# Performance work log

Hardware: AMD Instinct MI355X
Metric: run time of the kernel (lower is better)

The kernel has to match this reference:

```python
import jax, jax.numpy as jnp
import numpy as np

NUM_GRAPHS = 512


def _sage_conv(x, src, tgt, num_nodes, w_n, b_n, w_r):
    # PyG SAGEConv with mean aggregation:
    #   out = mean_{j in N(i)} x_j @ w_n + b_n + x_i @ w_r
    msgs = x[src]                                   # [E, d] gather
    agg = jax.ops.segment_sum(msgs, tgt, num_segments=num_nodes)   # [N, d]
    deg = jax.ops.segment_sum(jnp.ones((src.shape[0],), x.dtype), tgt,
                              num_segments=num_nodes)              # [N]
    agg = agg / jnp.maximum(deg, 1.0)[:, None]
    return agg @ w_n + b_n + x @ w_r


def setup_inputs() -> dict:
    key = jax.random.key(0)
    ks = jax.random.split(key, 10)
    N, E, D_IN, D_H, D_OUT = 50000, 800000, 128, 128, 10
    s = 0.05
    x = jax.random.normal(ks[0], (N, D_IN), dtype=jnp.float32)
    edge_index = jax.random.randint(ks[1], (2, E), 0, N, dtype=jnp.int64)
    batch = jnp.sort(jax.random.randint(ks[2], (N,), 0, NUM_GRAPHS, dtype=jnp.int64))
    return {
        "x": x,
        "edge_index": edge_index,
        "batch": batch,
        "w1_n": jax.random.normal(ks[3], (D_IN, D_H), dtype=jnp.float32) * s,
        "b1": jnp.zeros((D_H,), jnp.float32),
        "w1_r": jax.random.normal(ks[4], (D_IN, D_H), dtype=jnp.float32) * s,
        "w2_n": jax.random.normal(ks[5], (D_H, D_H), dtype=jnp.float32) * s,
        "b2": jnp.zeros((D_H,), jnp.float32),
        "w2_r": jax.random.normal(ks[6], (D_H, D_H), dtype=jnp.float32) * s,
        "fc_w": jax.random.normal(ks[7], (D_H, D_OUT), dtype=jnp.float32) * s,
        "fc_b": jnp.zeros((D_OUT,), jnp.float32),
    }


def reference(x, edge_index, batch, w1_n, b1, w1_r, w2_n, b2, w2_r, fc_w, fc_b):
    N = x.shape[0]
    src, tgt = edge_index[0], edge_index[1]
    h = _sage_conv(x, src, tgt, N, w1_n, b1, w1_r)
    h = jax.nn.relu(h)  # dropout is identity in eval mode
    h = _sage_conv(h, src, tgt, N, w2_n, b2, w2_r)
    # global_mean_pool over graph ids
    pooled = jax.ops.segment_sum(h, batch, num_segments=NUM_GRAPHS)
    cnt = jax.ops.segment_sum(jnp.ones((N,), h.dtype), batch, num_segments=NUM_GRAPHS)
    pooled = pooled / jnp.maximum(cnt, 1.0)[:, None]
    return pooled @ fc_w + fc_b
```

## Files before the change

kernel.cpp:

```cpp
#include <hip/hip_runtime.h>

#define D 128
#define G_NUM 512

typedef unsigned short u16;
typedef unsigned int u32;
typedef __attribute__((ext_vector_type(8))) short bf16x8;
typedef __attribute__((ext_vector_type(4))) float f32x4;

__device__ __forceinline__ float bf2f(u16 u) {
    return __uint_as_float(((u32)u) << 16);
}
__device__ __forceinline__ u16 f2bf_rne(float f) {
    u32 u = __float_as_uint(f);
    u32 r = (u + 0x7FFFu + ((u >> 16) & 1u)) >> 16;
    return (u16)r;
}
__device__ __forceinline__ void split_bf16(float v, u16& h, u16& l) {
    h = f2bf_rne(v);
    l = f2bf_rne(v - bf2f(h));
}
__device__ __forceinline__ float pk_hi(u32 u) { return __uint_as_float(u & 0xFFFF0000u); }
__device__ __forceinline__ float pk_lo(u32 u) { return __uint_as_float(u << 16); }
__device__ __forceinline__ bf16x8 mk8(u32 a, u32 b, u32 c, u32 d) {
    union { u32 u[4]; bf16x8 v; } t;
    t.u[0] = a; t.u[1] = b; t.u[2] = c; t.u[3] = d;
    return t.v;
}

__global__ void prep_kernel(const float* __restrict__ x, u16* __restrict__ xh, u16* __restrict__ xl,
                            const float* __restrict__ w0, const float* __restrict__ w1,
                            const float* __restrict__ w2, const float* __restrict__ w3,
                            u16* __restrict__ wp,
                            const int* __restrict__ batch, int* __restrict__ gstart,
                            const int* __restrict__ tgt, int* __restrict__ deg,
                            int n4, int E, int N, int NBX, int NBE) {
    int b = blockIdx.x, t = threadIdx.x;
    if (b < NBX) {
        int i = b * 256 + t;
        if (i >= n4) return;
        float4 v = ((const float4*)x)[i];
        ushort4 h, l;
        split_bf16(v.x, h.x, l.x);
        split_bf16(v.y, h.y, l.y);
        split_bf16(v.z, h.z, l.z);
        split_bf16(v.w, h.w, l.w);
        ((ushort4*)xh)[i] = h;
        ((ushort4*)xl)[i] = l;
    } else if (b < NBX + NBE) {
        int e = (b - NBX) * 256 + t;
        if (e < E) atomicAdd(&deg[tgt[e]], 1);
    } else if (b < NBX + NBE + 32) {
        int id = (b - NBX - NBE) * 256 + t;
        int g = id & 3, c = (id >> 2) & 127, kt = (id >> 9) & 3, mat = id >> 11;
        const float* W = (mat == 0) ? w0 : (mat == 1) ? w1 : (mat == 2) ? w2 : w3;
        u16* dh = wp + mat * 32768 + ((size_t)(kt * 128 + c) * 4 + g) * 8;
        u16* dl = dh + 16384;
#pragma unroll
        for (int j = 0; j < 8; j++) {
            float v = W[(size_t)(kt * 32 + g * 8 + j) * D + c];
            u16 h, l;
            split_bf16(v, h, l);
            dh[j] = h;
            dl[j] = l;
        }
    } else {
        int i = (b - NBX - NBE - 32) * 256 + t;
        if (i >= N) return;
        int bb = batch[i];
        int bp = (i == 0) ? -1 : batch[i - 1];
        for (int g = bp + 1; g <= bb; g++) gstart[g] = i;
        if (i == N - 1)
            for (int g = bb + 1; g <= G_NUM; g++) gstart[g] = N;
    }
}

__global__ void scan1_kernel(const int* __restrict__ deg, int* __restrict__ row_excl,
                             int* __restrict__ partial, int N) {
    __shared__ int s[256];
    int t = threadIdx.x, i = blockIdx.x * 256 + t;
    int v = (i < N) ? deg[i] : 0;
    s[t] = v;
    __syncthreads();
    for (int off = 1; off < 256; off <<= 1) {
        int add = (t >= off) ? s[t - off] : 0;
        __syncthreads();
        s[t] += add;
        __syncthreads();
    }
    if (i < N) row_excl[i] = s[t] - v;
    if (t == 255) partial[blockIdx.x] = s[255];
}

__global__ void scan2_kernel(int* __restrict__ partial, int NB) {
    __shared__ int s[256];
    int t = threadIdx.x;
    int v = (t < NB) ? partial[t] : 0;
    s[t] = v;
    __syncthreads();
    for (int off = 1; off < 256; off <<= 1) {
        int add = (t >= off) ? s[t - off] : 0;
        __syncthreads();
        s[t] += add;
        __syncthreads();
    }
    if (t < NB) partial[t] = s[t] - v;
}

__global__ void scan3_kernel(int* __restrict__ row_start, const int* __restrict__ partial,
                             int* __restrict__ deg, float* __restrict__ rdeg, int N, int E) {
    int i = blockIdx.x * blockDim.x + threadIdx.x;
    if (i < N) {
        row_start[i] += partial[blockIdx.x];
        float d = (float)deg[i];
        rdeg[i] = 1.0f / fmaxf(d, 1.0f);
        deg[i] = 0;
    }
    if (i == 0) row_start[N] = E;
}

__global__ void fill_kernel(const int* __restrict__ src, const int* __restrict__ tgt,
                            const int* __restrict__ row_start, int* __restrict__ cursor,
                            int* __restrict__ col_idx, int E) {
    int e = blockIdx.x * blockDim.x + threadIdx.x;
    if (e >= E) return;
    int t = tgt[e];
    int pos = row_start[t] + atomicAdd(&cursor[t], 1);
    col_idx[pos] = src[e];
}

template <int PK>
__global__ __launch_bounds__(256) void gather_kernel(
    const int* __restrict__ row_start, const int* __restrict__ col_idx,
    const float* __restrict__ rdeg, const void* __restrict__ feat,
    u16* __restrict__ agg_hi, u16* __restrict__ agg_lo, int N) {
    int node = blockIdx.x * 8 + (threadIdx.x >> 5);
    if (node >= N) return;
    int q = threadIdx.x & 31;
    int beg = row_start[node], end = row_start[node + 1];
    float ax = 0.f, ay = 0.f, az = 0.f, aw = 0.f;
    int i = beg;
    for (; i + 4 <= end; i += 4) {
        int s0 = col_idx[i], s1 = col_idx[i + 1], s2 = col_idx[i + 2], s3 = col_idx[i + 3];
        if (PK) {
            uint4 v0 = ((const uint4*)feat)[(size_t)s0 * 32 + q];
            uint4 v1 = ((const uint4*)feat)[(size_t)s1 * 32 + q];
            uint4 v2 = ((const uint4*)feat)[(size_t)s2 * 32 + q];
            uint4 v3 = ((const uint4*)feat)[(size_t)s3 * 32 + q];
            ax += (pk_hi(v0.x) + pk_lo(v0.x)) + (pk_hi(v1.x) + pk_lo(v1.x)) +
                  (pk_hi(v2.x) + pk_lo(v2.x)) + (pk_hi(v3.x) + pk_lo(v3.x));
            ay += (pk_hi(v0.y) + pk_lo(v0.y)) + (pk_hi(v1.y) + pk_lo(v1.y)) +
                  (pk_hi(v2.y) + pk_lo(v2.y)) + (pk_hi(v3.y) + pk_lo(v3.y));
            az += (pk_hi(v0.z) + pk_lo(v0.z)) + (pk_hi(v1.z) + pk_lo(v1.z)) +
                  (pk_hi(v2.z) + pk_lo(v2.z)) + (pk_hi(v3.z) + pk_lo(v3.z));
            aw += (pk_hi(v0.w) + pk_lo(v0.w)) + (pk_hi(v1.w) + pk_lo(v1.w)) +
                  (pk_hi(v2.w) + pk_lo(v2.w)) + (pk_hi(v3.w) + pk_lo(v3.w));
        } else {
            float4 v0 = ((const float4*)feat)[(size_t)s0 * 32 + q];
            float4 v1 = ((const float4*)feat)[(size_t)s1 * 32 + q];
            float4 v2 = ((const float4*)feat)[(size_t)s2 * 32 + q];
            float4 v3 = ((const float4*)feat)[(size_t)s3 * 32 + q];
            ax += v0.x + v1.x + v2.x + v3.x;
            ay += v0.y + v1.y + v2.y + v3.y;
            az += v0.z + v1.z + v2.z + v3.z;
            aw += v0.w + v1.w + v2.w + v3.w;
        }
    }
    for (; i < end; i++) {
        int s = col_idx[i];
        if (PK) {
            uint4 v = ((const uint4*)feat)[(size_t)s * 32 + q];
            ax += pk_hi(v.x) + pk_lo(v.x);
            ay += pk_hi(v.y) + pk_lo(v.y);
            az += pk_hi(v.z) + pk_lo(v.z);
            aw += pk_hi(v.w) + pk_lo(v.w);
        } else {
            float4 v = ((const float4*)feat)[(size_t)s * 32 + q];
            ax += v.x;
            ay += v.y;
            az += v.z;
            aw += v.w;
        }
    }
    float rd = rdeg[node];
    ax *= rd; ay *= rd; az *= rd; aw *= rd;
    ushort4 hv, lv;
    split_bf16(ax, hv.x, lv.x);
    split_bf16(ay, hv.y, lv.y);
    split_bf16(az, hv.z, lv.z);
    split_bf16(aw, hv.w, lv.w);
    *(ushort4*)(agg_hi + (size_t)node * D + q * 4) = hv;
    *(ushort4*)(agg_lo + (size_t)node * D + q * 4) = lv;
}

template <int XP, int OUTM>
__global__ __launch_bounds__(256, 2) void mfma_gemm_kernel(
    const u16* __restrict__ Ah, const u16* __restrict__ Al,
    const u16* __restrict__ Xh, const u16* __restrict__ Xl, const u32* __restrict__ Xp,
    const u16* __restrict__ Wnh, const u16* __restrict__ Wnl,
    const u16* __restrict__ Wrh, const u16* __restrict__ Wrl,
    const float* __restrict__ bias,
    u32* __restrict__ out_pk, float* __restrict__ out_f32, int N, int NT) {
    int wave = threadIdx.x >> 6;
    int lane = threadIdx.x & 63;
    int r = lane & 15, g = lane >> 4;
    int ctBase = wave * 2;

    bf16x8 Bn[2][4][2], Br[2][4][2];
#pragma unroll
    for (int c2 = 0; c2 < 2; c2++)
#pragma unroll
        for (int kt = 0; kt < 4; kt++) {
            size_t wo = ((size_t)(kt * 128 + r) * 4 + g) * 8 + (size_t)(ctBase + c2) * 512;
            Bn[c2][kt][0] = *(const bf16x8*)(Wnh + wo);
            Bn[c2][kt][1] = *(const bf16x8*)(Wnl + wo);
            Br[c2][kt][0] = *(const bf16x8*)(Wrh + wo);
            Br[c2][kt][1] = *(const bf16x8*)(Wrl + wo);
        }
    int col0 = ctBase * 16 + r, col1 = col0 + 16;
    float bv0 = bias[col0], bv1 = bias[col1];

    for (int rt = blockIdx.x; rt < NT; rt += gridDim.x) {
        int row0 = rt * 16;
        int arow = min(row0 + r, N - 1);
        size_t abase = (size_t)arow * D + g * 8;
        f32x4 acc0 = (f32x4){0.f, 0.f, 0.f, 0.f};
        f32x4 acc1 = (f32x4){0.f, 0.f, 0.f, 0.f};
#pragma unroll
        for (int kt = 0; kt < 4; kt++) {
            bf16x8 ah = *(const bf16x8*)(Ah + abase + kt * 32);
            bf16x8 al = *(const bf16x8*)(Al + abase + kt * 32);
            bf16x8 xh, xl;
            if (XP == 0) {
                xh = *(const bf16x8*)(Xh + abase + kt * 32);
                xl = *(const bf16x8*)(Xl + abase + kt * 32);
            } else {
                const u32* xp = Xp + abase + kt * 32;
                uint4 wa = *(const uint4*)(xp);
                uint4 wb = *(const uint4*)(xp + 4);
                xh = mk8((wa.y & 0xFFFF0000u) | (wa.x >> 16),
                         (wa.w & 0xFFFF0000u) | (wa.z >> 16),
                         (wb.y & 0xFFFF0000u) | (wb.x >> 16),
                         (wb.w & 0xFFFF0000u) | (wb.z >> 16));
                xl = mk8((wa.y << 16) | (wa.x & 0xFFFFu),
                         (wa.w << 16) | (wa.z & 0xFFFFu),
                         (wb.y << 16) | (wb.x & 0xFFFFu),
                         (wb.w << 16) | (wb.z & 0xFFFFu));
            }
            acc0 = __builtin_amdgcn_mfma_f32_16x16x32_bf16(ah, Bn[0][kt][0], acc0, 0, 0, 0);
            acc1 = __builtin_amdgcn_mfma_f32_16x16x32_bf16(ah, Bn[1][kt][0], acc1, 0, 0, 0);
            acc0 = __builtin_amdgcn_mfma_f32_16x16x32_bf16(al, Bn[0][kt][0], acc0, 0, 0, 0);
            acc1 = __builtin_amdgcn_mfma_f32_16x16x32_bf16(al, Bn[1][kt][0], acc1, 0, 0, 0);
            acc0 = __builtin_amdgcn_mfma_f32_16x16x32_bf16(ah, Bn[0][kt][1], acc0, 0, 0, 0);
            acc1 = __builtin_amdgcn_mfma_f32_16x16x32_bf16(ah, Bn[1][kt][1], acc1, 0, 0, 0);
            acc0 = __builtin_amdgcn_mfma_f32_16x16x32_bf16(xh, Br[0][kt][0], acc0, 0, 0, 0);
            acc1 = __builtin_amdgcn_mfma_f32_16x16x32_bf16(xh, Br[1][kt][0], acc1, 0, 0, 0);
            acc0 = __builtin_amdgcn_mfma_f32_16x16x32_bf16(xl, Br[0][kt][0], acc0, 0, 0, 0);
            acc1 = __builtin_amdgcn_mfma_f32_16x16x32_bf16(xl, Br[1][kt][0], acc1, 0, 0, 0);
            acc0 = __builtin_amdgcn_mfma_f32_16x16x32_bf16(xh, Br[0][kt][1], acc0, 0, 0, 0);
            acc1 = __builtin_amdgcn_mfma_f32_16x16x32_bf16(xh, Br[1][kt][1], acc1, 0, 0, 0);
        }
#pragma unroll
        for (int reg = 0; reg < 4; reg++) {
            int row = row0 + g * 4 + reg;
            if (row >= N) continue;
            float v0 = acc0[reg] + bv0;
            float v1 = acc1[reg] + bv1;
            if (OUTM == 0) {
                v0 = fmaxf(v0, 0.f);
                v1 = fmaxf(v1, 0.f);
                u16 h, l;
                split_bf16(v0, h, l);
                out_pk[(size_t)row * D + col0] = ((u32)h << 16) | l;
                split_bf16(v1, h, l);
                out_pk[(size_t)row * D + col1] = ((u32)h << 16) | l;
            } else {
                out_f32[(size_t)row * D + col0] = v0;
                out_f32[(size_t)row * D + col1] = v1;
            }
        }
    }
}

__global__ __launch_bounds__(128) void pool_fc_kernel(
    const float* __restrict__ h2, const int* __restrict__ gstart,
    const float* __restrict__ fcw, const float* __restrict__ fcb, float* __restrict__ out) {
    __shared__ float p[D];
    int g = blockIdx.x, t = threadIdx.x;
    int s = gstart[g], e = gstart[g + 1];
    float acc = 0.f;
    for (int r = s; r < e; r++) acc += h2[(size_t)r * D + t];
    float rc = 1.0f / fmaxf((float)(e - s), 1.0f);
    p[t] = acc * rc;
    __syncthreads();
    if (t < 10) {
        float o = fcb[t];
#pragma unroll
        for (int k = 0; k < D; k++) o += p[k] * fcw[k * 10 + t];
        out[g * 10 + t] = o;
    }
}

extern "C" void kernel_launch(void* const* d_in, const int* in_sizes, int n_in,
                              void* d_out, int out_size, void* d_ws, size_t ws_size,
                              hipStream_t stream) {
    const float* x   = (const float*)d_in[0];
    const int*   ei  = (const int*)d_in[1];
    const int* batch = (const int*)d_in[2];
    const float* w1n = (const float*)d_in[3];
    const float* b1  = (const float*)d_in[4];
    const float* w1r = (const float*)d_in[5];
    const float* w2n = (const float*)d_in[6];
    const float* b2  = (const float*)d_in[7];
    const float* w2r = (const float*)d_in[8];
    const float* fcw = (const float*)d_in[9];
    const float* fcb = (const float*)d_in[10];
    float* out = (float*)d_out;

    int N = in_sizes[0] / D;
    int E = in_sizes[1] / 2;
    const int* src = ei;
    const int* tgt = ei + E;
    int NB = (N + 255) / 256;

    auto au = [](size_t v) { return (v + 255) & ~(size_t)255; };
    char* p = (char*)d_ws;
    int*   deg       = (int*)p;    p += au((size_t)N * 4);
    int*   row_start = (int*)p;    p += au((size_t)(N + 1) * 4);
    int*   partial   = (int*)p;    p += au(256 * 4);
    int*   col_idx   = (int*)p;    p += au((size_t)E * 4);
    float* rdeg      = (float*)p;  p += au((size_t)N * 4);
    int*   gstart    = (int*)p;    p += au((size_t)(G_NUM + 1) * 4);
    u16*   wp        = (u16*)p;    p += au((size_t)8 * 16384 * 2);
    u16*   xh        = (u16*)p;    p += au((size_t)N * D * 2);
    u16*   xl        = (u16*)p;    p += au((size_t)N * D * 2);
    u16*   aggh      = (u16*)p;    p += au((size_t)N * D * 2);
    u16*   aggl      = (u16*)p;    p += au((size_t)N * D * 2);
    u32*   h1p       = (u32*)p;    p += au((size_t)N * D * 4);
    float* h2        = (float*)xh;

    hipMemsetAsync(deg, 0, (size_t)N * 4, stream);

    int n4 = N * 32;
    int NBX = (n4 + 255) / 256;
    int NBE = (E + 255) / 256;
    prep_kernel<<<NBX + NBE + 32 + NB, 256, 0, stream>>>(
        x, xh, xl, w1n, w1r, w2n, w2r, wp, batch, gstart, tgt, deg, n4, E, N, NBX, NBE);

    scan1_kernel<<<NB, 256, 0, stream>>>(deg, row_start, partial, N);
    scan2_kernel<<<1, 256, 0, stream>>>(partial, NB);
    scan3_kernel<<<NB, 256, 0, stream>>>(row_start, partial, deg, rdeg, N, E);
    fill_kernel<<<NBE, 256, 0, stream>>>(src, tgt, row_start, deg, col_idx, E);

    int gb = (N + 7) / 8;
    int NT = (N + 15) / 16;
    int gemm_grid = NT < 500 ? NT : 500;

    gather_kernel<0><<<gb, 256, 0, stream>>>(row_start, col_idx, rdeg, x, aggh, aggl, N);
    mfma_gemm_kernel<0, 0><<<gemm_grid, 256, 0, stream>>>(
        aggh, aggl, xh, xl, nullptr,
        wp + 0 * 32768, wp + 0 * 32768 + 16384,
        wp + 1 * 32768, wp + 1 * 32768 + 16384,
        b1, h1p, nullptr, N, NT);

    gather_kernel<1><<<gb, 256, 0, stream>>>(row_start, col_idx, rdeg, h1p, aggh, aggl, N);
    mfma_gemm_kernel<1, 1><<<gemm_grid, 256, 0, stream>>>(
        aggh, aggl, nullptr, nullptr, h1p,
        wp + 2 * 32768, wp + 2 * 32768 + 16384,
        wp + 3 * 32768, wp + 3 * 32768 + 16384,
        b2, nullptr, h2, N, NT);

    pool_fc_kernel<<<G_NUM, 128, 0, stream>>>(h2, gstart, fcw, fcb, out);
}
```

Before: 390.2 us.

## Fuse neighbor gather and MFMA GEMM into one persistent SAGE kernel per layer

Each SAGE layer's mean-aggregation gather and split-bf16 MFMA GEMM now run in a single persistent kernel. The aggregated 16-row tile is staged in LDS instead of written to global hi/lo buffers. Input x is stored once as packed hi/lo u32 words, so layer 1 gathers packed bf16 pairs instead of fp32. This removes the global round trip of the aggregation buffers and two launches, but the gather and GEMM phases now serialize within each block behind __syncthreads. Each wave computes only one 16-column tile, which may limit latency hiding for the irregular gathers.

After: 370.6 us. -5.0%, faster.

```diff
diff --git a/kernel.cpp b/kernel.cpp
--- a/kernel.cpp
+++ b/kernel.cpp
@@ -8,27 +8,32 @@
 typedef __attribute__((ext_vector_type(8))) short bf16x8;
 typedef __attribute__((ext_vector_type(4))) float f32x4;
 
-__device__ __forceinline__ float bf2f(u16 u) {
-    return __uint_as_float(((u32)u) << 16);
-}
+__device__ __forceinline__ float bf2f(u16 u) { return __uint_as_float(((u32)u) << 16); }
 __device__ __forceinline__ u16 f2bf_rne(float f) {
     u32 u = __float_as_uint(f);
-    u32 r = (u + 0x7FFFu + ((u >> 16) & 1u)) >> 16;
-    return (u16)r;
-}
-__device__ __forceinline__ void split_bf16(float v, u16& h, u16& l) {
-    h = f2bf_rne(v);
-    l = f2bf_rne(v - bf2f(h));
+    return (u16)((u + 0x7FFFu + ((u >> 16) & 1u)) >> 16);
+}
+__device__ __forceinline__ u32 packf(float v) {
+    u16 h = f2bf_rne(v);
+    u16 l = f2bf_rne(v - bf2f(h));
+    return ((u32)h << 16) | l;
 }
 __device__ __forceinline__ float pk_hi(u32 u) { return __uint_as_float(u & 0xFFFF0000u); }
 __device__ __forceinline__ float pk_lo(u32 u) { return __uint_as_float(u << 16); }
-__device__ __forceinline__ bf16x8 mk8(u32 a, u32 b, u32 c, u32 d) {
-    union { u32 u[4]; bf16x8 v; } t;
-    t.u[0] = a; t.u[1] = b; t.u[2] = c; t.u[3] = d;
-    return t.v;
-}
-
-__global__ void prep_kernel(const float* __restrict__ x, u16* __restrict__ xh, u16* __restrict__ xl,
+
+__device__ __forceinline__ void unpack8(const u32* w, bf16x8& hi, bf16x8& lo) {
+    union { u32 u[4]; bf16x8 v; } H, L;
+#pragma unroll
+    for (int p = 0; p < 4; p++) {
+        u32 a = w[2 * p], b = w[2 * p + 1];
+        H.u[p] = (b & 0xFFFF0000u) | (a >> 16);
+        L.u[p] = (b << 16) | (a & 0xFFFFu);
+    }
+    hi = H.v;
+    lo = L.v;
+}
+
+__global__ void prep_kernel(const float* __restrict__ x, u32* __restrict__ xp,
                             const float* __restrict__ w0, const float* __restrict__ w1,
                             const float* __restrict__ w2, const float* __restrict__ w3,
                             u16* __restrict__ wp,
@@ -40,13 +45,12 @@
         int i = b * 256 + t;
         if (i >= n4) return;
         float4 v = ((const float4*)x)[i];
-        ushort4 h, l;
-        split_bf16(v.x, h.x, l.x);
-        split_bf16(v.y, h.y, l.y);
-        split_bf16(v.z, h.z, l.z);
-        split_bf16(v.w, h.w, l.w);
-        ((ushort4*)xh)[i] = h;
-        ((ushort4*)xl)[i] = l;
+        uint4 o;
+        o.x = packf(v.x);
+        o.y = packf(v.y);
+        o.z = packf(v.z);
+        o.w = packf(v.w);
+        ((uint4*)xp)[i] = o;
     } else if (b < NBX + NBE) {
         int e = (b - NBX) * 256 + t;
         if (e < E) atomicAdd(&deg[tgt[e]], 1);
@@ -59,10 +63,9 @@
 #pragma unroll
         for (int j = 0; j < 8; j++) {
             float v = W[(size_t)(kt * 32 + g * 8 + j) * D + c];
-            u16 h, l;
-            split_bf16(v, h, l);
+            u16 h = f2bf_rne(v);
             dh[j] = h;
-            dl[j] = l;
+            dl[j] = f2bf_rne(v - bf2f(h));
         }
     } else {
         int i = (b - NBX - NBE - 32) * 256 + t;
@@ -129,156 +132,110 @@
     col_idx[pos] = src[e];
 }
 
-template <int PK>
-__global__ __launch_bounds__(256) void gather_kernel(
+template <int LAYER>
+__global__ __launch_bounds__(512, 4) void sage_fused_kernel(
     const int* __restrict__ row_start, const int* __restrict__ col_idx,
-    const float* __restrict__ rdeg, const void* __restrict__ feat,
-    u16* __restrict__ agg_hi, u16* __restrict__ agg_lo, int N) {
-    int node = blockIdx.x * 8 + (threadIdx.x >> 5);
-    if (node >= N) return;
-    int q = threadIdx.x & 31;
-    int beg = row_start[node], end = row_start[node + 1];
-    float ax = 0.f, ay = 0.f, az = 0.f, aw = 0.f;
-    int i = beg;
-    for (; i + 4 <= end; i += 4) {
-        int s0 = col_idx[i], s1 = col_idx[i + 1], s2 = col_idx[i + 2], s3 = col_idx[i + 3];
-        if (PK) {
-            uint4 v0 = ((const uint4*)feat)[(size_t)s0 * 32 + q];
-            uint4 v1 = ((const uint4*)feat)[(size_t)s1 * 32 + q];
-            uint4 v2 = ((const uint4*)feat)[(size_t)s2 * 32 + q];
-            uint4 v3 = ((const uint4*)feat)[(size_t)s3 * 32 + q];
-            ax += (pk_hi(v0.x) + pk_lo(v0.x)) + (pk_hi(v1.x) + pk_lo(v1.x)) +
-                  (pk_hi(v2.x) + pk_lo(v2.x)) + (pk_hi(v3.x) + pk_lo(v3.x));
-            ay += (pk_hi(v0.y) + pk_lo(v0.y)) + (pk_hi(v1.y) + pk_lo(v1.y)) +
-                  (pk_hi(v2.y) + pk_lo(v2.y)) + (pk_hi(v3.y) + pk_lo(v3.y));
-            az += (pk_hi(v0.z) + pk_lo(v0.z)) + (pk_hi(v1.z) + pk_lo(v1.z)) +
-                  (pk_hi(v2.z) + pk_lo(v2.z)) + (pk_hi(v3.z) + pk_lo(v3.z));
-            aw += (pk_hi(v0.w) + pk_lo(v0.w)) + (pk_hi(v1.w) + pk_lo(v1.w)) +
-                  (pk_hi(v2.w) + pk_lo(v2.w)) + (pk_hi(v3.w) + pk_lo(v3.w));
-        } else {
-            float4 v0 = ((const float4*)feat)[(size_t)s0 * 32 + q];
-            float4 v1 = ((const float4*)feat)[(size_t)s1 * 32 + q];
-            float4 v2 = ((const float4*)feat)[(size_t)s2 * 32 + q];
-            float4 v3 = ((const float4*)feat)[(size_t)s3 * 32 + q];
-            ax += v0.x + v1.x + v2.x + v3.x;
-            ay += v0.y + v1.y + v2.y + v3.y;
-            az += v0.z + v1.z + v2.z + v3.z;
-            aw += v0.w + v1.w + v2.w + v3.w;
-        }
-    }
-    for (; i < end; i++) {
-        int s = col_idx[i];
-        if (PK) {
-            uint4 v = ((const uint4*)feat)[(size_t)s * 32 + q];
-            ax += pk_hi(v.x) + pk_lo(v.x);
-            ay += pk_hi(v.y) + pk_lo(v.y);
-            az += pk_hi(v.z) + pk_lo(v.z);
-            aw += pk_hi(v.w) + pk_lo(v.w);
-        } else {
-            float4 v = ((const float4*)feat)[(size_t)s * 32 + q];
-            ax += v.x;
-            ay += v.y;
-            az += v.z;
-            aw += v.w;
-        }
-    }
-    float rd = rdeg[node];
-    ax *= rd; ay *= rd; az *= rd; aw *= rd;
-    ushort4 hv, lv;
-    split_bf16(ax, hv.x, lv.x);
-    split_bf16(ay, hv.y, lv.y);
-    split_bf16(az, hv.z, lv.z);
-    split_bf16(aw, hv.w, lv.w);
-    *(ushort4*)(agg_hi + (size_t)node * D + q * 4) = hv;
-    *(ushort4*)(agg_lo + (size_t)node * D + q * 4) = lv;
-}
-
-template <int XP, int OUTM>
-__global__ __launch_bounds__(256, 2) void mfma_gemm_kernel(
-    const u16* __restrict__ Ah, const u16* __restrict__ Al,
-    const u16* __restrict__ Xh, const u16* __restrict__ Xl, const u32* __restrict__ Xp,
+    const float* __restrict__ rdeg, const u32* __restrict__ feat_pk,
     const u16* __restrict__ Wnh, const u16* __restrict__ Wnl,
     const u16* __restrict__ Wrh, const u16* __restrict__ Wrl,
-    const float* __restrict__ bias,
-    u32* __restrict__ out_pk, float* __restrict__ out_f32, int N, int NT) {
-    int wave = threadIdx.x >> 6;
-    int lane = threadIdx.x & 63;
+    const float* __restrict__ bias, u32* __restrict__ out_pk,
+    float* __restrict__ out_f32, int N, int NT) {
+    __shared__ u32 agg[16 * 132];
+
+    int tid = threadIdx.x;
+    int lane = tid & 63;
+    int wave = tid >> 6;
     int r = lane & 15, g = lane >> 4;
-    int ctBase = wave * 2;
-
-    bf16x8 Bn[2][4][2], Br[2][4][2];
-#pragma unroll
-    for (int c2 = 0; c2 < 2; c2++)
+
+    bf16x8 Bn[4][2], Br[4][2];
+#pragma unroll
+    for (int kt = 0; kt < 4; kt++) {
+        size_t wo = ((size_t)(kt * 128 + r) * 4 + g) * 8 + (size_t)wave * 512;
+        Bn[kt][0] = *(const bf16x8*)(Wnh + wo);
+        Bn[kt][1] = *(const bf16x8*)(Wnl + wo);
+        Br[kt][0] = *(const bf16x8*)(Wrh + wo);
+        Br[kt][1] = *(const bf16x8*)(Wrl + wo);
+    }
+    float bv = bias[wave * 16 + r];
+
+    int nl = tid >> 5;
+    int q = tid & 31;
+
+    for (int rt = blockIdx.x; rt < NT; rt += gridDim.x) {
+        int node = rt * 16 + nl;
+        float ax = 0.f, ay = 0.f, az = 0.f, aw = 0.f;
+        if (node < N) {
+            int beg = row_start[node], end = row_start[node + 1];
+            int i = beg;
+            for (; i + 4 <= end; i += 4) {
+                int s0 = col_idx[i], s1 = col_idx[i + 1], s2 = col_idx[i + 2], s3 = col_idx[i + 3];
+                uint4 v0 = ((const uint4*)feat_pk)[(size_t)s0 * 32 + q];
+                uint4 v1 = ((const uint4*)feat_pk)[(size_t)s1 * 32 + q];
+                uint4 v2 = ((const uint4*)feat_pk)[(size_t)s2 * 32 + q];
+                uint4 v3 = ((const uint4*)feat_pk)[(size_t)s3 * 32 + q];
+                ax += (pk_hi(v0.x) + pk_lo(v0.x)) + (pk_hi(v1.x) + pk_lo(v1.x)) +
+                      (pk_hi(v2.x) + pk_lo(v2.x)) + (pk_hi(v3.x) + pk_lo(v3.x));
+                ay += (pk_hi(v0.y) + pk_lo(v0.y)) + (pk_hi(v1.y) + pk_lo(v1.y)) +
+                      (pk_hi(v2.y) + pk_lo(v2.y)) + (pk_hi(v3.y) + pk_lo(v3.y));
+                az += (pk_hi(v0.z) + pk_lo(v0.z)) + (pk_hi(v1.z) + pk_lo(v1.z)) +
+                      (pk_hi(v2.z) + pk_lo(v2.z)) + (pk_hi(v3.z) + pk_lo(v3.z));
+                aw += (pk_hi(v0.w) + pk_lo(v0.w)) + (pk_hi(v1.w) + pk_lo(v1.w)) +
+                      (pk_hi(v2.w) + pk_lo(v2.w)) + (pk_hi(v3.w) + pk_lo(v3.w));
+            }
+            for (; i < end; i++) {
+                int s = col_idx[i];
+                uint4 v = ((const uint4*)feat_pk)[(size_t)s * 32 + q];
+                ax += pk_hi(v.x) + pk_lo(v.x);
+                ay += pk_hi(v.y) + pk_lo(v.y);
+                az += pk_hi(v.z) + pk_lo(v.z);
+                aw += pk_hi(v.w) + pk_lo(v.w);
+            }
+            float rd = rdeg[node];
+            ax *= rd; ay *= rd; az *= rd; aw *= rd;
+        }
+        uint4 pk4;
+        pk4.x = packf(ax);
+        pk4.y = packf(ay);
+        pk4.z = packf(az);
+        pk4.w = packf(aw);
+        *(uint4*)&agg[nl * 132 + q * 4] = pk4;
+        __syncthreads();
+
+        int grow = min(rt * 16 + r, N - 1);
+        const u32* xrow = feat_pk + (size_t)grow * D;
+        f32x4 acc = (f32x4){0.f, 0.f, 0.f, 0.f};
 #pragma unroll
         for (int kt = 0; kt < 4; kt++) {
-            size_t wo = ((size_t)(kt * 128 + r) * 4 + g) * 8 + (size_t)(ctBase + c2) * 512;
-            Bn[c2][kt][0] = *(const bf16x8*)(Wnh + wo);
-            Bn[c2][kt][1] = *(const bf16x8*)(Wnl + wo);
-            Br[c2][kt][0] = *(const bf16x8*)(Wrh + wo);
-            Br[c2][kt][1] = *(const bf16x8*)(Wrl + wo);
+            u32 awb[8];
+            *(uint4*)&awb[0] = *(const uint4*)&agg[r * 132 + kt * 32 + g * 8];
+            *(uint4*)&awb[4] = *(const uint4*)&agg[r * 132 + kt * 32 + g * 8 + 4];
+            bf16x8 ah, al;
+            unpack8(awb, ah, al);
+            u32 xwb[8];
+            *(uint4*)&xwb[0] = *(const uint4*)(xrow + kt * 32 + g * 8);
+            *(uint4*)&xwb[4] = *(const uint4*)(xrow + kt * 32 + g * 8 + 4);
+            bf16x8 xh, xl;
+            unpack8(xwb, xh, xl);
+            acc = __builtin_amdgcn_mfma_f32_16x16x32_bf16(ah, Bn[kt][0], acc, 0, 0, 0);
+            acc = __builtin_amdgcn_mfma_f32_16x16x32_bf16(al, Bn[kt][0], acc, 0, 0, 0);
+            acc = __builtin_amdgcn_mfma_f32_16x16x32_bf16(ah, Bn[kt][1], acc, 0, 0, 0);
+            acc = __builtin_amdgcn_mfma_f32_16x16x32_bf16(xh, Br[kt][0], acc, 0, 0, 0);
+            acc = __builtin_amdgcn_mfma_f32_16x16x32_bf16(xl, Br[kt][0], acc, 0, 0, 0);
+            acc = __builtin_amdgcn_mfma_f32_16x16x32_bf16(xh, Br[kt][1], acc, 0, 0, 0);
         }
-    int col0 = ctBase * 16 + r, col1 = col0 + 16;
-    float bv0 = bias[col0], bv1 = bias[col1];
-
-    for (int rt = blockIdx.x; rt < NT; rt += gridDim.x) {
-        int row0 = rt * 16;
-        int arow = min(row0 + r, N - 1);
-        size_t abase = (size_t)arow * D + g * 8;
-        f32x4 acc0 = (f32x4){0.f, 0.f, 0.f, 0.f};
-        f32x4 acc1 = (f32x4){0.f, 0.f, 0.f, 0.f};
-#pragma unroll
-        for (int kt = 0; kt < 4; kt++) {
-            bf16x8 ah = *(const bf16x8*)(Ah + abase + kt * 32);
-            bf16x8 al = *(const bf16x8*)(Al + abase + kt * 32);
-            bf16x8 xh, xl;
-            if (XP == 0) {
-                xh = *(const bf16x8*)(Xh + abase + kt * 32);
-                xl = *(const bf16x8*)(Xl + abase + kt * 32);
+#pragma unroll
+        for (int reg = 0; reg < 4; reg++) {
+            int row = rt * 16 + g * 4 + reg;
+            if (row >= N) continue;
+            float v = acc[reg] + bv;
+            if (LAYER == 0) {
+                v = fmaxf(v, 0.f);
+                out_pk[(size_t)row * D + wave * 16 + r] = packf(v);
             } else {
-                const u32* xp = Xp + abase + kt * 32;
-                uint4 wa = *(const uint4*)(xp);
-                uint4 wb = *(const uint4*)(xp + 4);
-                xh = mk8((wa.y & 0xFFFF0000u) | (wa.x >> 16),
-                         (wa.w & 0xFFFF0000u) | (wa.z >> 16),
-                         (wb.y & 0xFFFF0000u) | (wb.x >> 16),
-                         (wb.w & 0xFFFF0000u) | (wb.z >> 16));
-                xl = mk8((wa.y << 16) | (wa.x & 0xFFFFu),
-                         (wa.w << 16) | (wa.z & 0xFFFFu),
-                         (wb.y << 16) | (wb.x & 0xFFFFu),
-                         (wb.w << 16) | (wb.z & 0xFFFFu));
-            }
-            acc0 = __builtin_amdgcn_mfma_f32_16x16x32_bf16(ah, Bn[0][kt][0], acc0, 0, 0, 0);
-            acc1 = __builtin_amdgcn_mfma_f32_16x16x32_bf16(ah, Bn[1][kt][0], acc1, 0, 0, 0);
-            acc0 = __builtin_amdgcn_mfma_f32_16x16x32_bf16(al, Bn[0][kt][0], acc0, 0, 0, 0);
-            acc1 = __builtin_amdgcn_mfma_f32_16x16x32_bf16(al, Bn[1][kt][0], acc1, 0, 0, 0);
-            acc0 = __builtin_amdgcn_mfma_f32_16x16x32_bf16(ah, Bn[0][kt][1], acc0, 0, 0, 0);
-            acc1 = __builtin_amdgcn_mfma_f32_16x16x32_bf16(ah, Bn[1][kt][1], acc1, 0, 0, 0);
-            acc0 = __builtin_amdgcn_mfma_f32_16x16x32_bf16(xh, Br[0][kt][0], acc0, 0, 0, 0);
-            acc1 = __builtin_amdgcn_mfma_f32_16x16x32_bf16(xh, Br[1][kt][0], acc1, 0, 0, 0);
-            acc0 = __builtin_amdgcn_mfma_f32_16x16x32_bf16(xl, Br[0][kt][0], acc0, 0, 0, 0);
-            acc1 = __builtin_amdgcn_mfma_f32_16x16x32_bf16(xl, Br[1][kt][0], acc1, 0, 0, 0);
-            acc0 = __builtin_amdgcn_mfma_f32_16x16x32_bf16(xh, Br[0][kt][1], acc0, 0, 0, 0);
-            acc1 = __builtin_amdgcn_mfma_f32_16x16x32_bf16(xh, Br[1][kt][1], acc1, 0, 0, 0);
-        }
-#pragma unroll
-        for (int reg = 0; reg < 4; reg++) {
-            int row = row0 + g * 4 + reg;
-            if (row >= N) continue;
-            float v0 = acc0[reg] + bv0;
-            float v1 = acc1[reg] + bv1;
-            if (OUTM == 0) {
-                v0 = fmaxf(v0, 0.f);
-                v1 = fmaxf(v1, 0.f);
-                u16 h, l;
-                split_bf16(v0, h, l);
-                out_pk[(size_t)row * D + col0] = ((u32)h << 16) | l;
-                split_bf16(v1, h, l);
-                out_pk[(size_t)row * D + col1] = ((u32)h << 16) | l;
-            } else {
-                out_f32[(size_t)row * D + col0] = v0;
-                out_f32[(size_t)row * D + col1] = v1;
+                out_f32[(size_t)row * D + wave * 16 + r] = v;
             }
         }
+        __syncthreads();
     }
 }
 
@@ -332,12 +289,9 @@
     float* rdeg      = (float*)p;  p += au((size_t)N * 4);
     int*   gstart    = (int*)p;    p += au((size_t)(G_NUM + 1) * 4);
     u16*   wp        = (u16*)p;    p += au((size_t)8 * 16384 * 2);
-    u16*   xh        = (u16*)p;    p += au((size_t)N * D * 2);
-    u16*   xl        = (u16*)p;    p += au((size_t)N * D * 2);
-    u16*   aggh      = (u16*)p;    p += au((size_t)N * D * 2);
-    u16*   aggl      = (u16*)p;    p += au((size_t)N * D * 2);
+    u32*   xp        = (u32*)p;    p += au((size_t)N * D * 4);
     u32*   h1p       = (u32*)p;    p += au((size_t)N * D * 4);
-    float* h2        = (float*)xh;
+    float* h2        = (float*)xp;
 
     hipMemsetAsync(deg, 0, (size_t)N * 4, stream);
 
@@ -345,27 +299,24 @@
     int NBX = (n4 + 255) / 256;
     int NBE = (E + 255) / 256;
     prep_kernel<<<NBX + NBE + 32 + NB, 256, 0, stream>>>(
-        x, xh, xl, w1n, w1r, w2n, w2r, wp, batch, gstart, tgt, deg, n4, E, N, NBX, NBE);
+        x, xp, w1n, w1r, w2n, w2r, wp, batch, gstart, tgt, deg, n4, E, N, NBX, NBE);
 
     scan1_kernel<<<NB, 256, 0, stream>>>(deg, row_start, partial, N);
     scan2_kernel<<<1, 256, 0, stream>>>(partial, NB);
     scan3_kernel<<<NB, 256, 0, stream>>>(row_start, partial, deg, rdeg, N, E);
     fill_kernel<<<NBE, 256, 0, stream>>>(src, tgt, row_start, deg, col_idx, E);
 
-    int gb = (N + 7) / 8;
     int NT = (N + 15) / 16;
-    int gemm_grid = NT < 500 ? NT : 500;
-
-    gather_kernel<0><<<gb, 256, 0, stream>>>(row_start, col_idx, rdeg, x, aggh, aggl, N);
-    mfma_gemm_kernel<0, 0><<<gemm_grid, 256, 0, stream>>>(
-        aggh, aggl, xh, xl, nullptr,
+    int grid = NT < 512 ? NT : 512;
+
+    sage_fused_kernel<0><<<grid, 512, 0, stream>>>(
+        row_start, col_idx, rdeg, xp,
         wp + 0 * 32768, wp + 0 * 32768 + 16384,
         wp + 1 * 32768, wp + 1 * 32768 + 16384,
         b1, h1p, nullptr, N, NT);
 
-    gather_kernel<1><<<gb, 256, 0, stream>>>(row_start, col_idx, rdeg, h1p, aggh, aggl, N);
-    mfma_gemm_kernel<1, 1><<<gemm_grid, 256, 0, stream>>>(
-        aggh, aggl, nullptr, nullptr, h1p,
+    sage_fused_kernel<1><<<grid, 512, 0, stream>>>(
+        row_start, col_idx, rdeg, h1p,
         wp + 2 * 32768, wp + 2 * 32768 + 16384,
         wp + 3 * 32768, wp + 3 * 32768 + 16384,
         b2, nullptr, h2, N, NT);
```
